# Optimization experiments

Hardware: AMD Instinct MI355X
Metric: run time of the kernel (lower is better)

## Reference

```python
import math
import jax, jax.numpy as jnp
from jax import lax
import numpy as np

B = 16384
L = 8          # hash levels
E = 8          # hash embedding dim per level
S = 16384      # hashmap size (2**14)
K = 32         # fourier frequencies
HID = 256
FF = 512       # fractal block inner dim (2*HID)
T = 48         # num_steps
ALPHA = 0.5
LAT = 32
VOCAB = 256
IN_DIM = 1 + 2 * K + L * E + LAT  # 161
PRIME1 = np.int32(73856093)
PRIME2 = 19349663


def _gelu(x):
    return jax.nn.gelu(x, approximate=False)  # torch nn.GELU default = exact erf


def setup_inputs() -> dict:
    key = jax.random.key(0)
    ks = jax.random.split(key, 16)
    x = jax.random.uniform(ks[0], (B,), dtype=jnp.float32)
    z = jax.random.normal(ks[1], (B, LAT), dtype=jnp.float32)
    hash_tables = jax.random.uniform(ks[2], (L, S, E), minval=-1e-4, maxval=1e-4, dtype=jnp.float32)

    def lin(k, fan_in, fan_out):
        bound = 1.0 / math.sqrt(fan_in)
        kw, kb = jax.random.split(k)
        W = jax.random.uniform(kw, (fan_in, fan_out), minval=-bound, maxval=bound, dtype=jnp.float32)
        b = jax.random.uniform(kb, (fan_out,), minval=-bound, maxval=bound, dtype=jnp.float32)
        return W, b

    W1, b1 = lin(ks[3], IN_DIM, HID)
    W2, b2 = lin(ks[4], HID, HID)
    Wf1, bf1 = lin(ks[5], HID, FF)
    Wf2, bf2 = lin(ks[6], FF, HID)
    Wo, bo = lin(ks[7], HID, VOCAB)

    resolutions = jnp.asarray(np.round(np.logspace(np.log10(16.0), np.log10(1024.0), L)).astype(np.int32))
    fourier_freqs = jnp.asarray(np.logspace(0.0, np.log10(10000.0), K).astype(np.float32))

    return dict(x=x, z=z, hash_tables=hash_tables, W1=W1, b1=b1, W2=W2, b2=b2,
                Wf1=Wf1, bf1=bf1, Wf2=Wf2, bf2=bf2, Wo=Wo, bo=bo,
                resolutions=resolutions, fourier_freqs=fourier_freqs)


def _forward(x, z, hash_tables, W1, b1, W2, b2, Wf1, bf1, Wf2, bf2, Wo, bo,
             resolutions, fourier_freqs):
    xn = jnp.clip(x, 0.0, 1.0)                              # [B]

    # Fourier features
    arg = (2.0 * math.pi) * xn[:, None] * fourier_freqs     # [B,K]
    four = jnp.concatenate([jnp.sin(arg), jnp.cos(arg)], axis=-1)  # [B,2K]

    # Hash grid (all levels vectorized)
    Rm1 = (resolutions - 1)                                  # [L] int32
    t = xn[:, None] * Rm1.astype(xn.dtype)                   # [B,L]
    i0 = jnp.floor(t).astype(jnp.int32)                      # [B,L]
    i1 = jnp.minimum(i0 + 1, Rm1)                            # [B,L]
    w = (t - i0.astype(xn.dtype))[..., None]                 # [B,L,1]
    lvl_term = (jnp.arange(L, dtype=jnp.int32) * jnp.int32(PRIME2))  # [L]
    h0 = jnp.mod(jnp.bitwise_xor(i0 * PRIME1, lvl_term), S)  # [B,L] (int32 wrap like torch)
    h1 = jnp.mod(jnp.bitwise_xor(i1 * PRIME1, lvl_term), S)
    lvl_idx = jnp.arange(L)[None, :]                         # [1,L]
    e0 = hash_tables[lvl_idx, h0]                            # [B,L,E]
    e1 = hash_tables[lvl_idx, h1]
    hfeat = (e0 * (1.0 - w) + e1 * w).reshape(xn.shape[0], L * E)  # [B,L*E]

    feats = jnp.concatenate([xn[:, None], four, hfeat, z], axis=-1)  # [B,161]

    h = _gelu(feats @ W1 + b1)
    h = _gelu(h @ W2 + b2)

    def step(h, _):
        u = jnp.tanh(_gelu(h @ Wf1 + bf1) @ Wf2 + bf2)
        return (1.0 - ALPHA) * h + ALPHA * u, None

    h, _ = lax.scan(step, h, None, length=T)
    return h @ Wo + bo                                       # [B,VOCAB]


def reference(x, z, hash_tables, W1, b1, W2, b2, Wf1, bf1, Wf2, bf2, Wo, bo,
              resolutions, fourier_freqs):
    return _forward(x, z, hash_tables, W1, b1, W2, b2, Wf1, bf1, Wf2, bf2, Wo, bo,
                    resolutions, fourier_freqs)
```

## Files before the change

### kernel.cpp

```cpp
#include <hip/hip_runtime.h>
#include <hip/hip_fp16.h>
#include <math.h>
#include <stdint.h>

typedef _Float16 f16;
typedef _Float16 h8 __attribute__((ext_vector_type(8)));
typedef float f4 __attribute__((ext_vector_type(4)));

#define TSTEPS 48

#define MFMA(a,b,c) __builtin_amdgcn_mfma_f32_16x16x32_f16((a),(b),(c),0,0,0)
#define MFMA_AB(acc, a, b) \
  asm("v_mfma_f32_16x16x32_f16 %0, %1, %2, %0" : "+a"(acc) : "v"(a), "a"(b))

__device__ __forceinline__ float gelu_f(float x) {
  float ax = fabsf(x) * 0.7071067811865475f;
  float t = __builtin_amdgcn_rcpf(1.0f + 0.3275911f * ax);
  float poly = t * (0.254829592f + t * (-0.284496736f + t * (1.421413741f +
               t * (-1.453152027f + t * 1.061405429f))));
  float e = exp2f(-ax * ax * 1.4426950408889634f);
  float er = copysignf(1.0f - poly * e, x);
  return 0.5f * x * (1.0f + er);
}

__device__ __forceinline__ float tanh_f(float x) {
  float e = exp2f(x * 2.885390081777927f);
  return 1.0f - 2.0f * __builtin_amdgcn_rcpf(e + 1.0f);
}

__device__ __forceinline__ void gload_lds16(const void* g, void* l) {
  __builtin_amdgcn_global_load_lds(
      (const __attribute__((address_space(1))) void*)g,
      (__attribute__((address_space(3))) void*)l, 16, 0, 0);
}

__global__ void prep_lin(const float* __restrict__ src, f16* __restrict__ dst,
                         int Kreal, int N, int total) {
  int idx = blockIdx.x * 256 + threadIdx.x;
  if (idx >= total) return;
  int fragid = idx >> 9;
  int within = idx & 511;
  int ln = within >> 3, e = within & 7;
  int nfr = N >> 4;
  int kk = fragid / nfr, cf = fragid - kk * nfr;
  int k = kk * 32 + ((ln >> 4) << 3) + e;
  int n = (cf << 4) + (ln & 15);
  dst[idx] = (f16)((k < Kreal) ? src[k * N + n] : 0.f);
}

__global__ void prep_wf1c(const float* __restrict__ src, f16* __restrict__ dst) {
  int idx = blockIdx.x * 256 + threadIdx.x;
  if (idx >= 131072) return;
  int f = idx >> 9, w = idx & 511;
  int ln = w >> 3, e = w & 7;
  int cf = f & 15, kk = (f >> 4) & 7, h = f >> 7;
  int n = 256 * h + 16 * cf + (ln & 15);
  int k = 32 * kk + 8 * (ln >> 4) + e;
  dst[idx] = (f16)src[k * 512 + n];
}

__global__ void feat_kernel(const float* __restrict__ x, const float* __restrict__ z,
                            const float* __restrict__ tables, const int* __restrict__ res,
                            const float* __restrict__ freqs, f16* __restrict__ featsH) {
  __shared__ f16 rowbuf[64][194];
  const int t = threadIdx.x;
  const int b = blockIdx.x;
  const int i = b * 64 + t;

  float xv = x[i];
  float xn = fminf(fmaxf(xv, 0.f), 1.f);
  f16* dst = rowbuf[t];
  dst[0] = (f16)xn;
  float w2pi = 6.283185307179586f * xn;
  #pragma unroll
  for (int k = 0; k < 32; ++k) {
    float a = w2pi * freqs[k];
    float s, c;
    sincosf(a, &s, &c);
    dst[1 + k]  = (f16)s;
    dst[33 + k] = (f16)c;
  }
  #pragma unroll
  for (int l = 0; l < 8; ++l) {
    int R = res[l];
    int Rm1 = R - 1;
    float tt = xn * (float)Rm1;
    int i0 = (int)tt;
    int i1 = min(i0 + 1, Rm1);
    float w = tt - (float)i0;
    uint32_t lt = (uint32_t)(l * 19349663);
    uint32_t h0 = (((uint32_t)i0 * 73856093u) ^ lt) & 16383u;
    uint32_t h1 = (((uint32_t)i1 * 73856093u) ^ lt) & 16383u;
    const float* e0 = tables + ((size_t)l * 16384 + h0) * 8;
    const float* e1 = tables + ((size_t)l * 16384 + h1) * 8;
    #pragma unroll
    for (int e = 0; e < 8; ++e) {
      float v = e0[e] * (1.f - w) + e1[e] * w;
      dst[65 + l * 8 + e] = (f16)v;
    }
  }
  #pragma unroll
  for (int j = 0; j < 32; ++j) dst[129 + j] = (f16)z[(size_t)i * 32 + j];
  #pragma unroll
  for (int j = 161; j < 192; ++j) dst[j] = (f16)0.f;

  __syncthreads();
  uint32_t* dg = (uint32_t*)(featsH + (size_t)b * 64 * 192);
  for (int idx = t; idx < 64 * 96; idx += 64) {
    int row = idx / 96, o = idx - row * 96;
    dg[idx] = ((const uint32_t*)&rowbuf[row][0])[o];
  }
}

__global__ __launch_bounds__(512)
__attribute__((amdgpu_waves_per_eu(2, 2)))
void fractal_main(
    const f16* __restrict__ featsH,
    const f16* __restrict__ W1L, const f16* __restrict__ W2L,
    const f16* __restrict__ WoL,
    const f16* __restrict__ Wf1C, const f16* __restrict__ Wf2L,
    const float* __restrict__ b1, const float* __restrict__ b2,
    const float* __restrict__ bf1, const float* __restrict__ bf2,
    const float* __restrict__ bo,
    float* __restrict__ out) {
  extern __shared__ char smem[];
  char* hB   = smem;
  char* uB   = smem + 32768;
  char* loB  = smem + 65536;
  char* wbuf = smem + 98304;

  const int tid = threadIdx.x;
  const int wn  = tid >> 6;
  const int ln  = tid & 63;
  const int r   = ln & 15;
  const int g   = ln >> 4;
  const int sw  = (r & 7) << 4;
  const int g16 = g * 16;
  const int row0 = blockIdx.x * 64;

  const int cH = 32 * wn + r;
  float b1r[2], b2r[2], bf2r[2], bor[2];
  #pragma unroll
  for (int nf = 0; nf < 2; ++nf) {
    b1r[nf] = b1[cH + 16 * nf]; b2r[nf] = b2[cH + 16 * nf];
    bf2r[nf] = bf2[cH + 16 * nf]; bor[nf] = bo[cH + 16 * nf];
  }
  float bf1r[2][2];
  #pragma unroll
  for (int h = 0; h < 2; ++h)
    #pragma unroll
    for (int nf = 0; nf < 2; ++nf)
      bf1r[h][nf] = bf1[256 * h + cH + 16 * nf];

  const f16* w1b  = W1L  + (2 * wn) * 512 + ln * 8;
  const f16* w2b  = W2L  + (2 * wn) * 512 + ln * 8;
  const f16* wob  = WoL  + (2 * wn) * 512 + ln * 8;
  const f16* wf2b = Wf2L + (2 * wn) * 512 + ln * 8;

  {
    const char* src = (const char*)featsH + (size_t)row0 * 384;
    for (int i = tid; i < 6144; i += 512) {
      int row = i / 96;
      int off = (i - row * 96) * 4;
      uint32_t v = *(const uint32_t*)(src + (size_t)i * 4);
      *(uint32_t*)(uB + row * 384 + (off ^ ((row & 7) << 4))) = v;
    }
  }
  __syncthreads();

  const f4 zf = {0.f, 0.f, 0.f, 0.f};

  {
    f4 acc[4][2];
    #pragma unroll
    for (int mf = 0; mf < 4; ++mf)
      #pragma unroll
      for (int nf = 0; nf < 2; ++nf) acc[mf][nf] = zf;
    #pragma unroll
    for (int kk = 0; kk < 6; ++kk) {
      h8 bb[2];
      #pragma unroll
      for (int nf = 0; nf < 2; ++nf)
        bb[nf] = *(const h8*)(w1b + ((size_t)(kk * 16 + nf) << 9));
      #pragma unroll
      for (int mf = 0; mf < 4; ++mf) {
        h8 a = *(const h8*)(uB + (16 * mf + r) * 384 + ((kk * 64 + g16) ^ sw));
        #pragma unroll
        for (int nf = 0; nf < 2; ++nf)
          acc[mf][nf] = MFMA(a, bb[nf], acc[mf][nf]);
      }
    }
    __syncthreads();
    #pragma unroll
    for (int mf = 0; mf < 4; ++mf)
      #pragma unroll
      for (int nf = 0; nf < 2; ++nf)
        #pragma unroll
        for (int j = 0; j < 4; ++j) {
          float hv = gelu_f(acc[mf][nf][j] + b1r[nf]);
          int row = 16 * mf + g * 4 + j;
          int col = cH + 16 * nf;
          *(f16*)(hB + row * 512 + ((col * 2) ^ ((row & 7) << 4))) = (f16)hv;
        }
  }
  __syncthreads();

  {
    f4 acc[4][2];
    #pragma unroll
    for (int mf = 0; mf < 4; ++mf)
      #pragma unroll
      for (int nf = 0; nf < 2; ++nf) acc[mf][nf] = zf;
    #pragma unroll
    for (int kk = 0; kk < 8; ++kk) {
      h8 bb[2];
      #pragma unroll
      for (int nf = 0; nf < 2; ++nf)
        bb[nf] = *(const h8*)(w2b + ((size_t)(kk * 16 + nf) << 9));
      #pragma unroll
      for (int mf = 0; mf < 4; ++mf) {
        h8 a = *(const h8*)(hB + (16 * mf + r) * 512 + ((kk * 64 + g16) ^ sw));
        #pragma unroll
        for (int nf = 0; nf < 2; ++nf)
          acc[mf][nf] = MFMA(a, bb[nf], acc[mf][nf]);
      }
    }
    __syncthreads();
    #pragma unroll
    for (int mf = 0; mf < 4; ++mf)
      #pragma unroll
      for (int nf = 0; nf < 2; ++nf)
        #pragma unroll
        for (int j = 0; j < 4; ++j) {
          float hv = gelu_f(acc[mf][nf][j] + b2r[nf]);
          int row = 16 * mf + g * 4 + j;
          int col = cH + 16 * nf;
          int so = (col * 2) ^ ((row & 7) << 4);
          f16 hi = (f16)hv;
          *(f16*)(hB + row * 512 + so) = hi;
          *(f16*)(loB + row * 512 + so) = (f16)(hv - (float)hi);
        }
  }
  __syncthreads();

  h8 wB[16][2];
  #pragma unroll
  for (int kk = 0; kk < 16; ++kk)
    #pragma unroll
    for (int nf = 0; nf < 2; ++nf) {
      wB[kk][nf] = *(const h8*)(wf2b + ((size_t)(kk * 16 + nf) << 9));
      asm("" : "+a"(wB[kk][nf]));
    }

  const char* wsrc = (const char*)Wf1C + wn * 2048 + ln * 16;
  char* wdst = wbuf + wn * 2048;
  #pragma unroll
  for (int c = 0; c < 2; ++c) {
    gload_lds16(wsrc + c * 16384, wdst + c * 16384);
    gload_lds16(wsrc + c * 16384 + 1024, wdst + c * 16384 + 1024);
  }
  int iad = 2, isl = 2, csl = 0;

  #pragma unroll 1
  for (int t = 0; t < TSTEPS; ++t) {
    f4 a2[4][2];
    #pragma unroll
    for (int mf = 0; mf < 4; ++mf)
      #pragma unroll
      for (int nf = 0; nf < 2; ++nf) a2[mf][nf] = zf;

    #pragma unroll
    for (int h = 0; h < 2; ++h) {
      f4 a1[4][2];
      #pragma unroll
      for (int mf = 0; mf < 4; ++mf)
        #pragma unroll
        for (int nf = 0; nf < 2; ++nf) a1[mf][nf] = zf;
      #pragma unroll 1
      for (int kk = 0; kk < 8; ++kk) {
        gload_lds16(wsrc + iad * 16384, wdst + isl * 16384);
        gload_lds16(wsrc + iad * 16384 + 1024, wdst + isl * 16384 + 1024);
        iad = (iad + 1) & 15;
        isl = (isl == 2) ? 0 : isl + 1;
        asm volatile("s_waitcnt vmcnt(4)" ::: "memory");
        __builtin_amdgcn_sched_barrier(0);
        const char* wb = wbuf + csl * 16384 + (2 * wn) * 1024 + ln * 16;
        csl = (csl == 2) ? 0 : csl + 1;
        h8 bb0 = *(const h8*)(wb);
        h8 bb1 = *(const h8*)(wb + 1024);
        #pragma unroll
        for (int mf = 0; mf < 4; ++mf) {
          h8 a = *(const h8*)(hB + (16 * mf + r) * 512 + ((kk * 64 + g16) ^ sw));
          a1[mf][0] = MFMA(a, bb0, a1[mf][0]);
          a1[mf][1] = MFMA(a, bb1, a1[mf][1]);
        }
      }
      #pragma unroll
      for (int mf = 0; mf < 4; ++mf)
        #pragma unroll
        for (int nf = 0; nf < 2; ++nf)
          #pragma unroll
          for (int j = 0; j < 4; ++j) {
            float gv = gelu_f(a1[mf][nf][j] + bf1r[h][nf]);
            int row = 16 * mf + g * 4 + j;
            int col = cH + 16 * nf;
            *(f16*)(uB + row * 512 + ((col * 2) ^ ((row & 7) << 4))) = (f16)gv;
          }
      __syncthreads();

      #pragma unroll
      for (int kk2 = 0; kk2 < 8; ++kk2) {
        #pragma unroll
        for (int mf = 0; mf < 4; ++mf) {
          h8 a = *(const h8*)(uB + (16 * mf + r) * 512 + ((kk2 * 64 + g16) ^ sw));
          MFMA_AB(a2[mf][0], a, wB[8 * h + kk2][0]);
          MFMA_AB(a2[mf][1], a, wB[8 * h + kk2][1]);
        }
      }
      __syncthreads();
    }

    #pragma unroll
    for (int mf = 0; mf < 4; ++mf)
      #pragma unroll
      for (int nf = 0; nf < 2; ++nf)
        #pragma unroll
        for (int j = 0; j < 4; ++j) {
          int row = 16 * mf + g * 4 + j;
          int col = cH + 16 * nf;
          int so = (col * 2) ^ ((row & 7) << 4);
          f16* hp = (f16*)(hB + row * 512 + so);
          f16* lp = (f16*)(loB + row * 512 + so);
          float mval = (float)*hp + (float)*lp;
          float u = tanh_f(a2[mf][nf][j] + bf2r[nf]);
          float hn = 0.5f * (mval + u);
          f16 hi = (f16)hn;
          *hp = hi;
          *lp = (f16)(hn - (float)hi);
        }
    __syncthreads();
  }

  {
    f4 acc[4][2];
    #pragma unroll
    for (int mf = 0; mf < 4; ++mf)
      #pragma unroll
      for (int nf = 0; nf < 2; ++nf) acc[mf][nf] = zf;
    #pragma unroll
    for (int kk = 0; kk < 8; ++kk) {
      h8 bb[2];
      #pragma unroll
      for (int nf = 0; nf < 2; ++nf)
        bb[nf] = *(const h8*)(wob + ((size_t)(kk * 16 + nf) << 9));
      #pragma unroll
      for (int mf = 0; mf < 4; ++mf) {
        h8 a = *(const h8*)(hB + (16 * mf + r) * 512 + ((kk * 64 + g16) ^ sw));
        #pragma unroll
        for (int nf = 0; nf < 2; ++nf)
          acc[mf][nf] = MFMA(a, bb[nf], acc[mf][nf]);
      }
    }
    #pragma unroll
    for (int mf = 0; mf < 4; ++mf)
      #pragma unroll
      for (int nf = 0; nf < 2; ++nf)
        #pragma unroll
        for (int j = 0; j < 4; ++j) {
          int row = row0 + 16 * mf + g * 4 + j;
          int col = cH + 16 * nf;
          out[(size_t)row * 256 + col] = acc[mf][nf][j] + bor[nf];
        }
  }
}

extern "C" void kernel_launch(void* const* d_in, const int* in_sizes, int n_in,
                              void* d_out, int out_size, void* d_ws, size_t ws_size,
                              hipStream_t stream) {
  const float* x      = (const float*)d_in[0];
  const float* z      = (const float*)d_in[1];
  const float* tables = (const float*)d_in[2];
  const float* W1     = (const float*)d_in[3];
  const float* b1     = (const float*)d_in[4];
  const float* W2     = (const float*)d_in[5];
  const float* b2     = (const float*)d_in[6];
  const float* Wf1    = (const float*)d_in[7];
  const float* bf1    = (const float*)d_in[8];
  const float* Wf2    = (const float*)d_in[9];
  const float* bf2    = (const float*)d_in[10];
  const float* Wo     = (const float*)d_in[11];
  const float* bo     = (const float*)d_in[12];
  const int*   res    = (const int*)d_in[13];
  const float* freqs  = (const float*)d_in[14];
  float* out = (float*)d_out;

  char* ws = (char*)d_ws;
  f16* featsH = (f16*)(ws);
  f16* W1L    = (f16*)(ws + 6291456);
  f16* W2L    = (f16*)(ws + 6389760);
  f16* WoL    = (f16*)(ws + 6520832);
  f16* Wf1C   = (f16*)(ws + 6651904);
  f16* Wf2L   = (f16*)(ws + 6914048);

  prep_lin<<<192, 256, 0, stream>>>(W1,  W1L,  161, 256, 96  * 512);
  prep_lin<<<256, 256, 0, stream>>>(W2,  W2L,  256, 256, 128 * 512);
  prep_lin<<<256, 256, 0, stream>>>(Wo,  WoL,  256, 256, 128 * 512);
  prep_wf1c<<<512, 256, 0, stream>>>(Wf1, Wf1C);
  prep_lin<<<512, 256, 0, stream>>>(Wf2, Wf2L, 512, 256, 256 * 512);
  feat_kernel<<<256, 64, 0, stream>>>(x, z, tables, res, freqs, featsH);

  (void)hipFuncSetAttribute((const void*)fractal_main,
                            hipFuncAttributeMaxDynamicSharedMemorySize, 147456);
  fractal_main<<<256, 512, 147456, stream>>>(featsH, W1L, W2L, WoL, Wf1C, Wf2L,
                                             b1, b2, bf1, bf2, bo, out);
}
```

Measured before the change: 970.2 us.

## Interleave second-half FF1 GEMM with first-half FF2 GEMM using double-buffered u

The per-step schedule is restructured so the second half of the Wf1 GEMM runs interleaved with the Wf2 GEMM on the first half's GELU output, using two separate u buffers. This removes two of the four block barriers per step. The Wf1 LDS streaming moves from a 3-slot ring to a fully unrolled 2-slot double buffer, prefetching one chunk ahead with vmcnt(2). Barriers become explicit lgkmcnt waits plus s_barrier. LDS use grows to 160KB, which leaves less headroom and gives a shallower prefetch distance.

```diff
diff --git a/kernel.cpp b/kernel.cpp
--- a/kernel.cpp
+++ b/kernel.cpp
@@ -32,6 +32,12 @@
   __builtin_amdgcn_global_load_lds(
       (const __attribute__((address_space(1))) void*)g,
       (__attribute__((address_space(3))) void*)l, 16, 0, 0);
+}
+
+__device__ __forceinline__ void barrier_lds() {
+  asm volatile("s_waitcnt lgkmcnt(0)" ::: "memory");
+  __builtin_amdgcn_s_barrier();
+  __builtin_amdgcn_sched_barrier(0);
 }
 
 __global__ void prep_lin(const float* __restrict__ src, f16* __restrict__ dst,
@@ -125,9 +131,10 @@
     float* __restrict__ out) {
   extern __shared__ char smem[];
   char* hB   = smem;
-  char* uB   = smem + 32768;
-  char* loB  = smem + 65536;
-  char* wbuf = smem + 98304;
+  char* loB  = smem + 32768;
+  char* uB0  = smem + 65536;
+  char* uB1  = smem + 98304;
+  char* wbuf = smem + 131072;
 
   const int tid = threadIdx.x;
   const int wn  = tid >> 6;
@@ -156,6 +163,9 @@
   const f16* w2b  = W2L  + (2 * wn) * 512 + ln * 8;
   const f16* wob  = WoL  + (2 * wn) * 512 + ln * 8;
   const f16* wf2b = Wf2L + (2 * wn) * 512 + ln * 8;
+  const char* wsrc = (const char*)Wf1C + wn * 2048 + ln * 16;
+  char* wdst = wbuf + wn * 2048;
+  const char* wcon = wbuf + wn * 2048 + ln * 16;
 
   {
     const char* src = (const char*)featsH + (size_t)row0 * 384;
@@ -163,7 +173,7 @@
       int row = i / 96;
       int off = (i - row * 96) * 4;
       uint32_t v = *(const uint32_t*)(src + (size_t)i * 4);
-      *(uint32_t*)(uB + row * 384 + (off ^ ((row & 7) << 4))) = v;
+      *(uint32_t*)(uB0 + row * 384 + (off ^ ((row & 7) << 4))) = v;
     }
   }
   __syncthreads();
@@ -184,7 +194,7 @@
         bb[nf] = *(const h8*)(w1b + ((size_t)(kk * 16 + nf) << 9));
       #pragma unroll
       for (int mf = 0; mf < 4; ++mf) {
-        h8 a = *(const h8*)(uB + (16 * mf + r) * 384 + ((kk * 64 + g16) ^ sw));
+        h8 a = *(const h8*)(uB0 + (16 * mf + r) * 384 + ((kk * 64 + g16) ^ sw));
         #pragma unroll
         for (int nf = 0; nf < 2; ++nf)
           acc[mf][nf] = MFMA(a, bb[nf], acc[mf][nf]);
@@ -252,14 +262,8 @@
       asm("" : "+a"(wB[kk][nf]));
     }
 
-  const char* wsrc = (const char*)Wf1C + wn * 2048 + ln * 16;
-  char* wdst = wbuf + wn * 2048;
-  #pragma unroll
-  for (int c = 0; c < 2; ++c) {
-    gload_lds16(wsrc + c * 16384, wdst + c * 16384);
-    gload_lds16(wsrc + c * 16384 + 1024, wdst + c * 16384 + 1024);
-  }
-  int iad = 2, isl = 2, csl = 0;
+  gload_lds16(wsrc, wdst);
+  gload_lds16(wsrc + 1024, wdst + 1024);
 
   #pragma unroll 1
   for (int t = 0; t < TSTEPS; ++t) {
@@ -269,23 +273,21 @@
       #pragma unroll
       for (int nf = 0; nf < 2; ++nf) a2[mf][nf] = zf;
 
-    #pragma unroll
-    for (int h = 0; h < 2; ++h) {
+    {
       f4 a1[4][2];
       #pragma unroll
       for (int mf = 0; mf < 4; ++mf)
         #pragma unroll
         for (int nf = 0; nf < 2; ++nf) a1[mf][nf] = zf;
-      #pragma unroll 1
+      #pragma unroll
       for (int kk = 0; kk < 8; ++kk) {
-        gload_lds16(wsrc + iad * 16384, wdst + isl * 16384);
-        gload_lds16(wsrc + iad * 16384 + 1024, wdst + isl * 16384 + 1024);
-        iad = (iad + 1) & 15;
-        isl = (isl == 2) ? 0 : isl + 1;
-        asm volatile("s_waitcnt vmcnt(4)" ::: "memory");
+        const int o = kk;
+        gload_lds16(wsrc + (((o + 1) & 15) << 14), wdst + (((o + 1) & 1) << 14));
+        gload_lds16(wsrc + (((o + 1) & 15) << 14) + 1024,
+                    wdst + (((o + 1) & 1) << 14) + 1024);
+        asm volatile("s_waitcnt vmcnt(2)" ::: "memory");
         __builtin_amdgcn_sched_barrier(0);
-        const char* wb = wbuf + csl * 16384 + (2 * wn) * 1024 + ln * 16;
-        csl = (csl == 2) ? 0 : csl + 1;
+        const char* wb = wcon + ((o & 1) << 14);
         h8 bb0 = *(const h8*)(wb);
         h8 bb1 = *(const h8*)(wb + 1024);
         #pragma unroll
@@ -301,25 +303,64 @@
         for (int nf = 0; nf < 2; ++nf)
           #pragma unroll
           for (int j = 0; j < 4; ++j) {
-            float gv = gelu_f(a1[mf][nf][j] + bf1r[h][nf]);
+            float gv = gelu_f(a1[mf][nf][j] + bf1r[0][nf]);
             int row = 16 * mf + g * 4 + j;
             int col = cH + 16 * nf;
-            *(f16*)(uB + row * 512 + ((col * 2) ^ ((row & 7) << 4))) = (f16)gv;
+            *(f16*)(uB0 + row * 512 + ((col * 2) ^ ((row & 7) << 4))) = (f16)gv;
           }
-      __syncthreads();
-
-      #pragma unroll
-      for (int kk2 = 0; kk2 < 8; ++kk2) {
+    }
+    barrier_lds();
+
+    {
+      f4 a1[4][2];
+      #pragma unroll
+      for (int mf = 0; mf < 4; ++mf)
+        #pragma unroll
+        for (int nf = 0; nf < 2; ++nf) a1[mf][nf] = zf;
+      #pragma unroll
+      for (int kk = 0; kk < 8; ++kk) {
+        const int o = 8 + kk;
+        gload_lds16(wsrc + (((o + 1) & 15) << 14), wdst + (((o + 1) & 1) << 14));
+        gload_lds16(wsrc + (((o + 1) & 15) << 14) + 1024,
+                    wdst + (((o + 1) & 1) << 14) + 1024);
+        asm volatile("s_waitcnt vmcnt(2)" ::: "memory");
+        __builtin_amdgcn_sched_barrier(0);
+        const char* wb = wcon + ((o & 1) << 14);
+        h8 bb0 = *(const h8*)(wb);
+        h8 bb1 = *(const h8*)(wb + 1024);
         #pragma unroll
         for (int mf = 0; mf < 4; ++mf) {
-          h8 a = *(const h8*)(uB + (16 * mf + r) * 512 + ((kk2 * 64 + g16) ^ sw));
-          MFMA_AB(a2[mf][0], a, wB[8 * h + kk2][0]);
-          MFMA_AB(a2[mf][1], a, wB[8 * h + kk2][1]);
-        }
-      }
-      __syncthreads();
-    }
-
+          h8 aH = *(const h8*)(hB + (16 * mf + r) * 512 + ((kk * 64 + g16) ^ sw));
+          a1[mf][0] = MFMA(aH, bb0, a1[mf][0]);
+          a1[mf][1] = MFMA(aH, bb1, a1[mf][1]);
+          h8 aU = *(const h8*)(uB0 + (16 * mf + r) * 512 + ((kk * 64 + g16) ^ sw));
+          MFMA_AB(a2[mf][0], aU, wB[kk][0]);
+          MFMA_AB(a2[mf][1], aU, wB[kk][1]);
+        }
+      }
+      #pragma unroll
+      for (int mf = 0; mf < 4; ++mf)
+        #pragma unroll
+        for (int nf = 0; nf < 2; ++nf)
+          #pragma unroll
+          for (int j = 0; j < 4; ++j) {
+            float gv = gelu_f(a1[mf][nf][j] + bf1r[1][nf]);
+            int row = 16 * mf + g * 4 + j;
+            int col = cH + 16 * nf;
+            *(f16*)(uB1 + row * 512 + ((col * 2) ^ ((row & 7) << 4))) = (f16)gv;
+          }
+    }
+    barrier_lds();
+
+    #pragma unroll
+    for (int kk = 0; kk < 8; ++kk) {
+      #pragma unroll
+      for (int mf = 0; mf < 4; ++mf) {
+        h8 aU = *(const h8*)(uB1 + (16 * mf + r) * 512 + ((kk * 64 + g16) ^ sw));
+        MFMA_AB(a2[mf][0], aU, wB[8 + kk][0]);
+        MFMA_AB(a2[mf][1], aU, wB[8 + kk][1]);
+      }
+    }
     #pragma unroll
     for (int mf = 0; mf < 4; ++mf)
       #pragma unroll
@@ -338,7 +379,7 @@
           *hp = hi;
           *lp = (f16)(hn - (float)hi);
         }
-    __syncthreads();
+    barrier_lds();
   }
 
   {
@@ -410,7 +451,7 @@
   feat_kernel<<<256, 64, 0, stream>>>(x, z, tables, res, freqs, featsH);
 
   (void)hipFuncSetAttribute((const void*)fractal_main,
-                            hipFuncAttributeMaxDynamicSharedMemorySize, 147456);
-  fractal_main<<<256, 512, 147456, stream>>>(featsH, W1L, W2L, WoL, Wf1C, Wf2L,
+                            hipFuncAttributeMaxDynamicSharedMemorySize, 163840);
+  fractal_main<<<256, 512, 163840, stream>>>(featsH, W1L, W2L, WoL, Wf1C, Wf2L,
                                              b1, b2, bf1, bf2, bo, out);
 }
```

New measurement: 1.553 ms. +60.1%, slower.
